# Optimization experiments

Measured on AMD Instinct MI355X. Metric: run time of the kernel, lower is better.

The kernel has to match this reference:

```python
import jax, jax.numpy as jnp
import numpy as np

# ---- sedenion multiplication table via Cayley-Dickson construction ----
def _cd_conj(x):
    if x.shape[0] == 1:
        return x
    h = x.shape[0] // 2
    return np.concatenate([_cd_conj(x[:h]), -x[h:]])

def _cd_mult(x, y):
    n = x.shape[0]
    if n == 1:
        return x * y
    h = n // 2
    a, b = x[:h], x[h:]
    c, d = y[:h], y[h:]
    return np.concatenate([
        _cd_mult(a, c) - _cd_mult(_cd_conj(d), b),
        _cd_mult(d, a) + _cd_mult(b, _cd_conj(c)),
    ])

def _sed_table():
    T = np.zeros((16, 16, 16), dtype=np.float32)
    I = np.eye(16, dtype=np.float32)
    for i in range(16):
        for j in range(16):
            r = _cd_mult(I[i], I[j])  # e_i * e_j = sign * e_k
            k = int(np.abs(r).argmax())
            T[i, j, k] = r[k]
    return T

_T = jnp.asarray(_sed_table())  # [16,16,16] constant sign table

DIM = 128
MLP_RATIO = 4
EPS = 1e-5

def _ln(x, g, b):
    m = jnp.mean(x, axis=-1, keepdims=True)
    v = jnp.mean((x - m) ** 2, axis=-1, keepdims=True)
    return (x - m) * jax.lax.rsqrt(v + EPS) * g + b

def setup_inputs() -> dict:
    key = jax.random.key(0)
    ks = jax.random.split(key, 8)
    C, Ch = DIM, DIM * MLP_RATIO
    s = 1.0 / np.sqrt(C)
    inp = {
        "x": jax.random.normal(ks[0], (8, C, 128, 128), dtype=jnp.float32),
        "gamma1": jnp.ones((C,), jnp.float32),
        "beta1": jnp.zeros((C,), jnp.float32),
        "sed_w": jax.random.normal(ks[1], (16, C, C), jnp.float32) * (s / 4.0),
        "w_proj": jax.random.normal(ks[2], (C, C), jnp.float32) * s,
        "b_proj": jnp.zeros((C,), jnp.float32),
        "gamma2": jnp.ones((C,), jnp.float32),
        "beta2": jnp.zeros((C,), jnp.float32),
        "w1": jax.random.normal(ks[3], (C, Ch), jnp.float32) * s,
        "b1": jnp.zeros((Ch,), jnp.float32),
        "w2": jax.random.normal(ks[4], (Ch, C), jnp.float32) * (1.0 / np.sqrt(Ch)),
        "b2": jnp.zeros((C,), jnp.float32),
    }
    return inp

def reference(x, gamma1, beta1, sed_w, w_proj, b_proj, gamma2, beta2, w1, b1, w2, b2):
    B, C, H, W = x.shape  # H, W divisible by 4 -> no padding branch
    h, w = H // 4, W // 4
    xt = jnp.transpose(x, (0, 2, 3, 1))          # [B,H,W,C]
    # norm1
    xn = _ln(xt, gamma1, beta1)
    # window partition: 'b c (h s1)(w s2) -> b h w (s1 s2 c)'
    xw = xn.reshape(B, h, 4, w, 4, C).transpose(0, 1, 3, 2, 4, 5).reshape(B, h, w, 16, C)
    # SedenionLinear: y_k = sum_{i,j} T[i,j,k] * x_i @ W_j  (bias=False)
    ys = jnp.einsum('bhwic,ijk,jcd->bhwkd', xw, _T, sed_w)
    # reverse window + to bhwc
    y = ys.reshape(B, h, w, 4, 4, C).transpose(0, 1, 3, 2, 4, 5).reshape(B, H, W, C)
    # act + proj
    y = jax.nn.gelu(y, approximate=False)
    y = y @ w_proj + b_proj
    # residual 1
    y = xt + y
    # norm2 + MLP + residual 2
    m = _ln(y, gamma2, beta2)
    m = jax.nn.gelu(m @ w1 + b1, approximate=False)
    m = m @ w2 + b2
    out = y + m
    return jnp.transpose(out, (0, 3, 1, 2))  # back to [B,C,H,W]
```

## Files before the change

### kernel.cpp

```cpp
#include <hip/hip_runtime.h>
#include <hip/hip_bf16.h>

#define DEVI __device__ __forceinline__

typedef __attribute__((ext_vector_type(8))) __bf16 bf16x8;
typedef __attribute__((ext_vector_type(4))) __bf16 bf16x4;
typedef __attribute__((ext_vector_type(4))) float f32x4;

using bf16 = __hip_bfloat16;

DEVI float bf2f(bf16 v) { return __bfloat162float(v); }
DEVI bf16 f2bf(float v) { return __float2bfloat16(v); }

DEVI float gelu_fast(float v) {
    float t = v * (2.30220777f + 0.10294322f * v * v);
    float e = __builtin_amdgcn_exp2f(t);
    return v - v * __builtin_amdgcn_rcpf(e + 1.0f);
}

DEVI void async16(void* lds, const void* g) {
    __builtin_amdgcn_global_load_lds(
        (const __attribute__((address_space(1))) void*)g,
        (__attribute__((address_space(3))) void*)lds, 16, 0, 0);
}

DEVI int cd_sign(int i, int j) {
    int s = 1, n = 16;
    while (n > 1) {
        int h = n >> 1;
        int ih = (i >= h), jh = (j >= h);
        if (!ih && !jh) {
        } else if (!ih && jh) {
            int ni = j - h, nj = i;
            i = ni; j = nj;
        } else if (ih && !jh) {
            if (j != 0) s = -s;
            i = i - h;
        } else {
            int ni = j - h, nj = i - h;
            if (ni == 0) s = -s;
            i = ni; j = nj;
        }
        n = h;
    }
    return s;
}

__global__ __launch_bounds__(256) void k_prep_A(const float* __restrict__ sed_w,
                                                bf16* __restrict__ At) {
    __shared__ float tile[128][129];
    int bi = blockIdx.x;
    int i = bi >> 4, k = bi & 15;
    int j = i ^ k;
    float s = (float)cd_sign(i, j);
    int t = threadIdx.x;
    int lo = t & 127, hi = t >> 7;
    const float* src = sed_w + j * 16384;
    for (int it = 0; it < 64; ++it) {
        int c = it * 2 + hi;
        tile[c][lo] = src[c * 128 + lo];
    }
    __syncthreads();
    for (int it = 0; it < 64; ++it) {
        int d = it * 2 + hi;
        At[(long)(k * 128 + d) * 2048 + i * 128 + lo] = f2bf(s * tile[lo][d]);
    }
}

__global__ __launch_bounds__(256) void k_prep_w(const float* __restrict__ wp,
                                                const float* __restrict__ w1,
                                                const float* __restrict__ w2,
                                                bf16* __restrict__ wpT,
                                                bf16* __restrict__ w1T,
                                                bf16* __restrict__ w2T) {
    int idx = blockIdx.x * 256 + threadIdx.x;
    if (idx < 16384) {
        int d = idx >> 7, c = idx & 127;
        wpT[idx] = f2bf(wp[c * 128 + d]);
    } else if (idx < 16384 + 65536) {
        int e = idx - 16384;
        int o = e >> 7, c = e & 127;
        w1T[e] = f2bf(w1[c * 512 + o]);
    } else if (idx < 16384 + 131072) {
        int e = idx - 81920;
        int o = e >> 9, c = e & 511;
        w2T[e] = f2bf(w2[c * 128 + o]);
    }
}

__global__ __launch_bounds__(256) void k_ln1(const float* __restrict__ x,
                                             const float* __restrict__ g,
                                             const float* __restrict__ bta,
                                             bf16* __restrict__ xt,
                                             bf16* __restrict__ xn) {
    __shared__ float tile[128][128];
    __shared__ float ps[2][128], pss[2][128];
    int b = blockIdx.x >> 7, r = blockIdx.x & 127;
    int t = threadIdx.x, c = t & 127, half = t >> 7;
    const float* xb = x + ((long)b * 128 * 128 + r) * 128;
    for (int it = 0; it < 64; ++it) {
        int ch = it * 2 + half;
        tile[ch][c] = xb[(long)ch * 16384 + c];
    }
    __syncthreads();
    float s = 0.f, ss = 0.f;
    for (int ch = half * 64; ch < half * 64 + 64; ++ch) {
        float v = tile[ch][c];
        s += v; ss += v * v;
    }
    ps[half][c] = s; pss[half][c] = ss;
    __syncthreads();
    float S = ps[0][c] + ps[1][c], SS = pss[0][c] + pss[1][c];
    float mean = S * (1.f / 128.f);
    float var = SS * (1.f / 128.f) - mean * mean;
    float rstd = rsqrtf(var + 1e-5f);
    long n = (((long)b * 32 + (r >> 2)) * 32 + (c >> 2)) * 16 + ((r & 3) * 4 + (c & 3));
    bf16* xtr = xt + n * 128 + half * 64;
    bf16* xnr = xn + n * 128 + half * 64;
#pragma unroll
    for (int v8 = 0; v8 < 8; ++v8) {
        bf16x8 pt, pn;
#pragma unroll
        for (int e = 0; e < 8; ++e) {
            int ch = half * 64 + v8 * 8 + e;
            float v = tile[ch][c];
            pt[e] = (__bf16)v;
            pn[e] = (__bf16)((v - mean) * rstd * g[ch] + bta[ch]);
        }
        *(bf16x8*)&xtr[v8 * 8] = pt;
        *(bf16x8*)&xnr[v8 * 8] = pn;
    }
}

__global__ __launch_bounds__(256, 3) void k_gemm_sed(const bf16* __restrict__ At,
                                                     const bf16* __restrict__ xn,
                                                     bf16* __restrict__ g_) {
    const int K = 2048;
    __shared__ __align__(16) char buf[34816];
    bf16* lA = (bf16*)buf;
    bf16* lB = (bf16*)(buf + 8192);
    bf16* sOut = (bf16*)buf;
    int t = threadIdx.x;
    long bm = (long)blockIdx.y * 128;
    long bn = (long)blockIdx.x * 128;
    int lane = t & 63;
    int wm = ((t >> 7) & 1) * 64;
    int wn = ((t >> 6) & 1) * 64;
    int l15 = lane & 15, quad = lane >> 4;

    f32x4 acc[4][4] = {};

    int rowA = t >> 2;
    int seg = (t & 3) * 8;
    const bf16* gA = At + (bm + rowA) * (long)K + seg;
    const bf16* gB = xn + (bn + rowA) * (long)K + seg;

    for (int k0 = 0; k0 < K; k0 += 32) {
        async16(&lA[t * 8], gA + k0);
        async16(&lA[2048 + t * 8], gA + (long)64 * K + k0);
        async16(&lB[t * 8], gB + k0);
        async16(&lB[2048 + t * 8], gB + (long)64 * K + k0);
        __syncthreads();
        bf16x8 af[4], bfr[4];
#pragma unroll
        for (int tm = 0; tm < 4; ++tm)
            af[tm] = *(const bf16x8*)&lA[(wm + tm * 16 + l15) * 32 + quad * 8];
#pragma unroll
        for (int tn = 0; tn < 4; ++tn)
            bfr[tn] = *(const bf16x8*)&lB[(wn + tn * 16 + l15) * 32 + quad * 8];
#pragma unroll
        for (int tm = 0; tm < 4; ++tm)
#pragma unroll
            for (int tn = 0; tn < 4; ++tn)
                acc[tm][tn] = __builtin_amdgcn_mfma_f32_16x16x32_bf16(
                    af[tm], bfr[tn], acc[tm][tn], 0, 0, 0);
        __syncthreads();
    }

#pragma unroll
    for (int tn = 0; tn < 4; ++tn) {
        int win = wn + tn * 16 + l15;
#pragma unroll
        for (int tm = 0; tm < 4; ++tm) {
            int kd = wm + tm * 16 + quad * 4;
            bf16x4 p;
#pragma unroll
            for (int reg = 0; reg < 4; ++reg)
                p[reg] = (__bf16)gelu_fast(acc[tm][tn][reg]);
            *(bf16x4*)&sOut[win * 136 + kd] = p;
        }
    }
    __syncthreads();
#pragma unroll
    for (int it = 0; it < 8; ++it) {
        int id = it * 256 + t;
        int win = id >> 4, sg = id & 15;
        bf16x8 v = *(const bf16x8*)&sOut[win * 136 + sg * 8];
        *(bf16x8*)&g_[(bn + win) * 2048 + bm + sg * 8] = v;
    }
}

__global__ __launch_bounds__(256, 2) void k_tail(
    const bf16* __restrict__ g_,
    const bf16* __restrict__ wpT,
    const float* __restrict__ bproj,
    const bf16* __restrict__ xt,
    const float* __restrict__ gamma2, const float* __restrict__ beta2,
    const bf16* __restrict__ w1T,
    const float* __restrict__ b1,
    const bf16* __restrict__ w2T,
    const float* __restrict__ b2,
    float* __restrict__ out)
{
    __shared__ __align__(16) char buf[71680];
    bf16* mpT = (bf16*)buf;
    float* stats = (float*)(buf + 34816);
    float* outF = (float*)buf;

    int t = threadIdx.x;
    long tb = (long)blockIdx.x * 128;
    int lane = t & 63;
    int wm = ((t >> 7) & 1) * 64;
    int wm1 = ((t >> 7) & 1) * 32;
    int wn = ((t >> 6) & 1) * 64;
    int l15 = lane & 15, quad = lane >> 4;
    int half = wm >> 6;

    int tok[4];
#pragma unroll
    for (int tn = 0; tn < 4; ++tn) tok[tn] = wn + tn * 16 + l15;

    f32x4 acc1[4][4] = {};
#pragma unroll
    for (int k0 = 0; k0 < 128; k0 += 32) {
        bf16x8 af[4], bfr[4];
#pragma unroll
        for (int tm = 0; tm < 4; ++tm)
            af[tm] = *(const bf16x8*)&wpT[(wm + tm * 16 + l15) * 128 + k0 + quad * 8];
#pragma unroll
        for (int tn = 0; tn < 4; ++tn)
            bfr[tn] = *(const bf16x8*)&g_[(tb + tok[tn]) * 128 + k0 + quad * 8];
#pragma unroll
        for (int tm = 0; tm < 4; ++tm)
#pragma unroll
            for (int tn = 0; tn < 4; ++tn)
                acc1[tm][tn] = __builtin_amdgcn_mfma_f32_16x16x32_bf16(
                    af[tm], bfr[tn], acc1[tm][tn], 0, 0, 0);
    }

#pragma unroll
    for (int tm = 0; tm < 4; ++tm) {
        int c0 = wm + tm * 16 + quad * 4;
        float4 bp = *(const float4*)&bproj[c0];
#pragma unroll
        for (int tn = 0; tn < 4; ++tn) {
            bf16x4 xv = *(const bf16x4*)&xt[(tb + tok[tn]) * 128 + c0];
#pragma unroll
            for (int reg = 0; reg < 4; ++reg)
                acc1[tm][tn][reg] += ((const float*)&bp)[reg] + (float)xv[reg];
        }
    }

#pragma unroll
    for (int tn = 0; tn < 4; ++tn) {
        float s = 0.f, ss = 0.f;
#pragma unroll
        for (int tm = 0; tm < 4; ++tm)
#pragma unroll
            for (int reg = 0; reg < 4; ++reg) {
                float v = acc1[tm][tn][reg];
                s += v; ss += v * v;
            }
        s += __shfl_xor(s, 16); ss += __shfl_xor(ss, 16);
        s += __shfl_xor(s, 32); ss += __shfl_xor(ss, 32);
        if (quad == 0) {
            stats[tok[tn] * 2 + half] = s;
            stats[256 + tok[tn] * 2 + half] = ss;
        }
    }
    __syncthreads();

    float mean[4], rstd[4];
#pragma unroll
    for (int tn = 0; tn < 4; ++tn) {
        float S = stats[tok[tn] * 2] + stats[tok[tn] * 2 + 1];
        float SS = stats[256 + tok[tn] * 2] + stats[256 + tok[tn] * 2 + 1];
        mean[tn] = S * (1.f / 128.f);
        float var = SS * (1.f / 128.f) - mean[tn] * mean[tn];
        rstd[tn] = rsqrtf(var + 1e-5f);
    }
#pragma unroll
    for (int tm = 0; tm < 4; ++tm) {
        int c0 = wm + tm * 16 + quad * 4;
        float4 gv = *(const float4*)&gamma2[c0];
        float4 bv = *(const float4*)&beta2[c0];
#pragma unroll
        for (int tn = 0; tn < 4; ++tn) {
            bf16x4 p;
#pragma unroll
            for (int reg = 0; reg < 4; ++reg)
                p[reg] = (__bf16)((acc1[tm][tn][reg] - mean[tn]) * rstd[tn] *
                                      ((const float*)&gv)[reg] +
                                  ((const float*)&bv)[reg]);
            *(bf16x4*)&mpT[tok[tn] * 136 + c0] = p;
        }
    }
    __syncthreads();

    f32x4 acc2[4][4] = {};
    for (int oh = 0; oh < 8; ++oh) {
        bf16* hT = (bf16*)(buf + 34816 + (oh & 1) * 18432);
        f32x4 acch[2][4] = {};
#pragma unroll
        for (int k0 = 0; k0 < 128; k0 += 32) {
            bf16x8 af[2], bfr[4];
#pragma unroll
            for (int tm = 0; tm < 2; ++tm)
                af[tm] = *(const bf16x8*)&w1T[(oh * 64 + wm1 + tm * 16 + l15) * 128 +
                                              k0 + quad * 8];
#pragma unroll
            for (int tn = 0; tn < 4; ++tn)
                bfr[tn] = *(const bf16x8*)&mpT[tok[tn] * 136 + k0 + quad * 8];
#pragma unroll
            for (int tm = 0; tm < 2; ++tm)
#pragma unroll
                for (int tn = 0; tn < 4; ++tn)
                    acch[tm][tn] = __builtin_amdgcn_mfma_f32_16x16x32_bf16(
                        af[tm], bfr[tn], acch[tm][tn], 0, 0, 0);
        }
#pragma unroll
        for (int tm = 0; tm < 2; ++tm) {
            int hc0 = wm1 + tm * 16 + quad * 4;
            float4 bh = *(const float4*)&b1[oh * 64 + hc0];
#pragma unroll
            for (int tn = 0; tn < 4; ++tn) {
                bf16x4 p;
#pragma unroll
                for (int reg = 0; reg < 4; ++reg)
                    p[reg] = (__bf16)gelu_fast(acch[tm][tn][reg] +
                                               ((const float*)&bh)[reg]);
                *(bf16x4*)&hT[tok[tn] * 72 + hc0] = p;
            }
        }
        __syncthreads();
#pragma unroll
        for (int k0 = 0; k0 < 64; k0 += 32) {
            bf16x8 af[4], bfr[4];
#pragma unroll
            for (int tm = 0; tm < 4; ++tm)
                af[tm] = *(const bf16x8*)&w2T[(wm + tm * 16 + l15) * 512 +
                                              oh * 64 + k0 + quad * 8];
#pragma unroll
            for (int tn = 0; tn < 4; ++tn)
                bfr[tn] = *(const bf16x8*)&hT[tok[tn] * 72 + k0 + quad * 8];
#pragma unroll
            for (int tm = 0; tm < 4; ++tm)
#pragma unroll
                for (int tn = 0; tn < 4; ++tn)
                    acc2[tm][tn] = __builtin_amdgcn_mfma_f32_16x16x32_bf16(
                        af[tm], bfr[tn], acc2[tm][tn], 0, 0, 0);
        }
    }
    __syncthreads();

    long win0 = tb >> 4;
    int b = (int)(win0 >> 10);
    int hq = (int)(win0 >> 5) & 31;
    int wq0 = (int)win0 & 31;
#pragma unroll
    for (int p = 0; p < 2; ++p) {
#pragma unroll
        for (int tmi = 0; tmi < 2; ++tmi) {
            int tm = p * 2 + tmi;
            int c0 = wm + tm * 16 + quad * 4;
            int slot0 = (wm >> 1) + tmi * 16 + quad * 4;
            float4 bv = *(const float4*)&b2[c0];
#pragma unroll
            for (int tn = 0; tn < 4; ++tn)
#pragma unroll
                for (int reg = 0; reg < 4; ++reg)
                    outF[(slot0 + reg) * 132 + tok[tn]] =
                        acc1[tm][tn][reg] + acc2[tm][tn][reg] +
                        ((const float*)&bv)[reg];
        }
        __syncthreads();
#pragma unroll
        for (int it = 0; it < 8; ++it) {
            int id = it * 256 + t;
            int slot = id >> 5, rem = id & 31;
            int rr = rem >> 3, wqo = rem & 7;
            int c = slot + ((slot >= 32) ? 32 : 0) + p * 32;
            f32x4 v = *(const f32x4*)&outF[slot * 132 + wqo * 16 + rr * 4];
            long addr = (((long)b * 128 + c) * 128 + hq * 4 + rr) * 128 +
                        (wq0 + wqo) * 4;
            *(f32x4*)&out[addr] = v;
        }
        __syncthreads();
    }
}

extern "C" void kernel_launch(void* const* d_in, const int* in_sizes, int n_in,
                              void* d_out, int out_size, void* d_ws, size_t ws_size,
                              hipStream_t stream) {
    const float* x      = (const float*)d_in[0];
    const float* gamma1 = (const float*)d_in[1];
    const float* beta1  = (const float*)d_in[2];
    const float* sed_w  = (const float*)d_in[3];
    const float* w_proj = (const float*)d_in[4];
    const float* b_proj = (const float*)d_in[5];
    const float* gamma2 = (const float*)d_in[6];
    const float* beta2  = (const float*)d_in[7];
    const float* w1     = (const float*)d_in[8];
    const float* b1     = (const float*)d_in[9];
    const float* w2     = (const float*)d_in[10];
    const float* b2     = (const float*)d_in[11];

    char* ws = (char*)d_ws;
    bf16* At  = (bf16*)(ws + 0);
    bf16* wpT = (bf16*)(ws + 8388608);
    bf16* w1T = (bf16*)(ws + 8421376);
    bf16* w2T = (bf16*)(ws + 8552448);
    bf16* xt  = (bf16*)(ws + 8683520);
    bf16* xn  = (bf16*)(ws + 42237952);
    bf16* g_  = (bf16*)(ws + 75792384);

    hipLaunchKernelGGL(k_prep_w, dim3(576), dim3(256), 0, stream,
                       w_proj, w1, w2, wpT, w1T, w2T);
    hipLaunchKernelGGL(k_prep_A, dim3(256), dim3(256), 0, stream, sed_w, At);
    hipLaunchKernelGGL(k_ln1, dim3(1024), dim3(256), 0, stream,
                       x, gamma1, beta1, xt, xn);
    hipLaunchKernelGGL(k_gemm_sed, dim3(64, 16), dim3(256), 0, stream,
                       At, xn, g_);
    hipLaunchKernelGGL(k_tail, dim3(1024), dim3(256), 0, stream,
                       g_, wpT, b_proj, xt, gamma2, beta2,
                       w1T, b1, w2T, b2, (float*)d_out);
}
```

Measured before the change: 347.6 us.

## Rewrite sedenion GEMM with 256x256 tiles, double-buffered async loads and swizzled LDS

The sedenion GEMM moves from 128x128 tiles with 256 threads to 256x256 tiles with 512 threads (8 waves) and a 64-wide K step. Global-to-LDS async loads are double-buffered with explicit vmcnt waits, so the next stage's loads overlap the current MFMA work. An XOR swizzle on the LDS layout avoids bank conflicts, and s_setprio is raised around the MFMA bursts. The cost is 128KB of dynamic LDS, more barriers per K step, larger accumulator register pressure, and a grid of only 256 blocks, which may leave some CUs idle.

```diff
diff --git a/kernel.cpp b/kernel.cpp
--- a/kernel.cpp
+++ b/kernel.cpp
@@ -132,71 +132,128 @@
     }
 }
 
-__global__ __launch_bounds__(256, 3) void k_gemm_sed(const bf16* __restrict__ At,
+__global__ __launch_bounds__(512, 2) void k_gemm_sed(const bf16* __restrict__ At,
                                                      const bf16* __restrict__ xn,
                                                      bf16* __restrict__ g_) {
-    const int K = 2048;
-    __shared__ __align__(16) char buf[34816];
-    bf16* lA = (bf16*)buf;
-    bf16* lB = (bf16*)(buf + 8192);
+    extern __shared__ __align__(16) char buf[];
+    const int t = threadIdx.x;
+    const long bn = (long)blockIdx.x * 256;
+    const long bm = (long)blockIdx.y * 256;
+    const int lane = t & 63;
+    const int wid = t >> 6;
+    const int wm2 = wid >> 2;
+    const int wn4 = wid & 3;
+    const int l15 = lane & 15, quad = lane >> 4;
+
+    const int srow = t >> 3;
+    const int sslot = (t & 7) ^ (srow & 7);
+    const bf16* gA0 = At + (bm + srow) * 2048L + sslot * 8;
+    const bf16* gB0 = xn + (bn + srow) * 2048L + sslot * 8;
+
+    char* const ldsA = buf;
+    char* const ldsB = buf + 65536;
+
+    const int ax0 = ((quad + 0) ^ (l15 & 7)) << 4;
+    const int ax1 = ((quad + 4) ^ (l15 & 7)) << 4;
+    const int aRowBase = wm2 * 16384 + l15 * 128;
+    const int bRowBase = (wn4 >> 1) * 16384 + ((wn4 & 1) * 64 + l15) * 128;
+
+#define SED_STAGE(d, kt)                                                     \
+    {                                                                        \
+        const long k0_ = (long)(kt) * 64;                                    \
+        char* la_ = ldsA + (d) * 32768;                                      \
+        char* lb_ = ldsB + (d) * 32768;                                      \
+        const bf16* ga_ = gA0 + k0_;                                         \
+        const bf16* gb_ = gB0 + k0_;                                         \
+        _Pragma("unroll")                                                    \
+        for (int h_ = 0; h_ < 2; ++h_)                                       \
+            _Pragma("unroll")                                                \
+            for (int r_ = 0; r_ < 2; ++r_) {                                 \
+                const long gro_ = (long)(h_ * 128 + r_ * 64) * 2048;         \
+                const int lo_ = h_ * 16384 + r_ * 8192 + t * 16;             \
+                async16(la_ + lo_, ga_ + gro_);                              \
+                async16(lb_ + lo_, gb_ + gro_);                              \
+            }                                                                \
+    }
+
+    SED_STAGE(0, 0);
+    SED_STAGE(1, 1);
+
+    f32x4 acc[8][4] = {};
+
+    for (int tt = 0; tt < 32; ++tt) {
+        const int d = tt & 1;
+        if (tt < 31) asm volatile("s_waitcnt vmcnt(8)" ::: "memory");
+        else         asm volatile("s_waitcnt vmcnt(0)" ::: "memory");
+        __builtin_amdgcn_s_barrier();
+        asm volatile("" ::: "memory");
+
+        char* const la = ldsA + d * 32768 + aRowBase;
+        char* const lb = ldsB + d * 32768 + bRowBase;
+#pragma unroll
+        for (int p = 0; p < 4; ++p) {
+            const int kk = p & 1, mh = p >> 1;
+            const int xo = kk ? ax1 : ax0;
+            bf16x8 af[4], bfr[4];
+#pragma unroll
+            for (int i = 0; i < 4; ++i)
+                af[i] = *(const bf16x8*)(la + (mh * 4 + i) * 2048 + xo);
+#pragma unroll
+            for (int n = 0; n < 4; ++n)
+                bfr[n] = *(const bf16x8*)(lb + n * 2048 + xo);
+            __builtin_amdgcn_s_barrier();
+            __builtin_amdgcn_s_setprio(1);
+#pragma unroll
+            for (int i = 0; i < 4; ++i)
+#pragma unroll
+                for (int n = 0; n < 4; ++n)
+                    acc[mh * 4 + i][n] = __builtin_amdgcn_mfma_f32_16x16x32_bf16(
+                        af[i], bfr[n], acc[mh * 4 + i][n], 0, 0, 0);
+            __builtin_amdgcn_s_setprio(0);
+            __builtin_amdgcn_s_barrier();
+        }
+        if (tt < 30) {
+            asm volatile("" ::: "memory");
+            SED_STAGE(d, tt + 2);
+        }
+    }
+#undef SED_STAGE
+
+    __syncthreads();
     bf16* sOut = (bf16*)buf;
-    int t = threadIdx.x;
-    long bm = (long)blockIdx.y * 128;
-    long bn = (long)blockIdx.x * 128;
-    int lane = t & 63;
-    int wm = ((t >> 7) & 1) * 64;
-    int wn = ((t >> 6) & 1) * 64;
-    int l15 = lane & 15, quad = lane >> 4;
-
-    f32x4 acc[4][4] = {};
-
-    int rowA = t >> 2;
-    int seg = (t & 3) * 8;
-    const bf16* gA = At + (bm + rowA) * (long)K + seg;
-    const bf16* gB = xn + (bn + rowA) * (long)K + seg;
-
-    for (int k0 = 0; k0 < K; k0 += 32) {
-        async16(&lA[t * 8], gA + k0);
-        async16(&lA[2048 + t * 8], gA + (long)64 * K + k0);
-        async16(&lB[t * 8], gB + k0);
-        async16(&lB[2048 + t * 8], gB + (long)64 * K + k0);
+#pragma unroll
+    for (int p2 = 0; p2 < 2; ++p2) {
+        if (wm2 == p2) {
+#pragma unroll
+            for (int m = 0; m < 8; ++m)
+#pragma unroll
+                for (int n = 0; n < 4; ++n) {
+                    int win = wn4 * 64 + n * 16 + l15;
+                    int kdl = m * 16 + quad * 4;
+                    bf16x4 v;
+#pragma unroll
+                    for (int r = 0; r < 4; ++r)
+                        v[r] = (__bf16)gelu_fast(acc[m][n][r]);
+                    int slot = kdl >> 3;
+                    int off = win * 256 + ((slot ^ (win & 7)) << 4) +
+                              ((kdl * 2) & 15);
+                    *(bf16x4*)((char*)sOut + off) = v;
+                }
+        }
         __syncthreads();
-        bf16x8 af[4], bfr[4];
-#pragma unroll
-        for (int tm = 0; tm < 4; ++tm)
-            af[tm] = *(const bf16x8*)&lA[(wm + tm * 16 + l15) * 32 + quad * 8];
-#pragma unroll
-        for (int tn = 0; tn < 4; ++tn)
-            bfr[tn] = *(const bf16x8*)&lB[(wn + tn * 16 + l15) * 32 + quad * 8];
-#pragma unroll
-        for (int tm = 0; tm < 4; ++tm)
-#pragma unroll
-            for (int tn = 0; tn < 4; ++tn)
-                acc[tm][tn] = __builtin_amdgcn_mfma_f32_16x16x32_bf16(
-                    af[tm], bfr[tn], acc[tm][tn], 0, 0, 0);
+#pragma unroll
+        for (int rr = 0; rr < 2; ++rr) {
+            int win = (t >> 2) + rr * 128;
+            int sub = t & 3;
+#pragma unroll
+            for (int j = 0; j < 4; ++j) {
+                int c = j * 4 + sub;
+                bf16x8 v = *(const bf16x8*)((char*)sOut + win * 256 +
+                                            ((c ^ (win & 7)) << 4));
+                *(bf16x8*)&g_[(bn + win) * 2048L + bm + p2 * 128 + c * 8] = v;
+            }
+        }
         __syncthreads();
-    }
-
-#pragma unroll
-    for (int tn = 0; tn < 4; ++tn) {
-        int win = wn + tn * 16 + l15;
-#pragma unroll
-        for (int tm = 0; tm < 4; ++tm) {
-            int kd = wm + tm * 16 + quad * 4;
-            bf16x4 p;
-#pragma unroll
-            for (int reg = 0; reg < 4; ++reg)
-                p[reg] = (__bf16)gelu_fast(acc[tm][tn][reg]);
-            *(bf16x4*)&sOut[win * 136 + kd] = p;
-        }
-    }
-    __syncthreads();
-#pragma unroll
-    for (int it = 0; it < 8; ++it) {
-        int id = it * 256 + t;
-        int win = id >> 4, sg = id & 15;
-        bf16x8 v = *(const bf16x8*)&sOut[win * 136 + sg * 8];
-        *(bf16x8*)&g_[(bn + win) * 2048 + bm + sg * 8] = v;
     }
 }
 
@@ -429,7 +486,7 @@
     hipLaunchKernelGGL(k_prep_A, dim3(256), dim3(256), 0, stream, sed_w, At);
     hipLaunchKernelGGL(k_ln1, dim3(1024), dim3(256), 0, stream,
                        x, gamma1, beta1, xt, xn);
-    hipLaunchKernelGGL(k_gemm_sed, dim3(64, 16), dim3(256), 0, stream,
+    hipLaunchKernelGGL(k_gemm_sed, dim3(32, 8), dim3(512), 131072, stream,
                        At, xn, g_);
     hipLaunchKernelGGL(k_tail, dim3(1024), dim3(256), 0, stream,
                        g_, wpT, b_proj, xt, gamma2, beta2,
```

Measured after the change: 335.6 us. 3.5% less time.
